# Optimization experiments

Measured on AMD Instinct MI355X. Metric: run time of the kernel, lower is better.

Reference implementation:

```python
import jax, jax.numpy as jnp
import numpy as np

B, S, N, E = 8, 32, 2000, 64000
GH, H = 32, 64  # gat_h, lstm hidden
NEG_SLOPE = 0.2


def setup_inputs() -> dict:
    key = jax.random.key(0)
    ks = jax.random.split(key, 12)
    f32 = jnp.float32
    x = jax.random.normal(ks[0], (B, S, N), f32)
    edge_index = jax.random.randint(ks[1], (2, E), 0, N)
    # GATConv(1, GH, heads=1, concat=False): lin weight [GH,1] -> vector, att_src/att_dst [GH], bias [GH]
    w_lin = jax.random.normal(ks[2], (GH,), f32)
    att_src = jax.random.normal(ks[3], (GH,), f32) * 0.1
    att_dst = jax.random.normal(ks[4], (GH,), f32) * 0.1
    gat_bias = jax.random.normal(ks[5], (GH,), f32) * 0.01
    D = GH * N  # LSTM input size
    W_ih = jax.random.normal(ks[6], (4 * H, D), f32) * (1.0 / np.sqrt(D))
    W_hh = jax.random.normal(ks[7], (4 * H, H), f32) * (1.0 / np.sqrt(H))
    b_ih = jax.random.normal(ks[8], (4 * H,), f32) * 0.01
    b_hh = jax.random.normal(ks[9], (4 * H,), f32) * 0.01
    W_head = jax.random.normal(ks[10], (N, H), f32) * (1.0 / np.sqrt(H))
    b_head = jax.random.normal(ks[11], (N,), f32) * 0.01
    return {"x": x, "edge_index": edge_index, "w_lin": w_lin, "att_src": att_src,
            "att_dst": att_dst, "gat_bias": gat_bias, "W_ih": W_ih, "W_hh": W_hh,
            "b_ih": b_ih, "b_hh": b_hh, "W_head": W_head, "b_head": b_head}


def reference(x, edge_index, w_lin, att_src, att_dst, gat_bias,
              W_ih, W_hh, b_ih, b_hh, W_head, b_head):
    x = x.astype(jnp.float32)
    # --- GAT (in_channels=1, heads=1), batched over (B,S) ---
    # PyG default: add self-loops
    loops = jnp.arange(N)
    ei = jnp.concatenate([edge_index, jnp.stack([loops, loops])], axis=1)
    src, dst = ei[0], ei[1]  # [Et], Et = E + N
    # lifted feature h_n = x_n * w_lin (rank-1), so attention logits are scalar per node
    a_src = x * jnp.dot(w_lin, att_src)  # [B,S,N]
    a_dst = x * jnp.dot(w_lin, att_dst)  # [B,S,N]
    e = jax.nn.leaky_relu(a_src[..., src] + a_dst[..., dst], NEG_SLOPE)  # [B,S,Et]
    e = jnp.moveaxis(e, -1, 0)  # [Et,B,S] (segment axis leading)
    seg_max = jax.ops.segment_max(e, dst, num_segments=N)  # [N,B,S]
    e = jnp.exp(e - seg_max[dst])
    denom = jax.ops.segment_sum(e, dst, num_segments=N)  # [N,B,S]
    alpha = e / denom[dst]  # edge softmax over incoming edges
    x_src = jnp.moveaxis(x[..., src], -1, 0)  # [Et,B,S]
    agg = jax.ops.segment_sum(alpha * x_src, dst, num_segments=N)  # [N,B,S]
    agg = jnp.moveaxis(agg, 0, -1)  # [B,S,N]
    # outer product with w_lin restores [.,GH]; add bias, then relu (from forward)
    h = jax.nn.relu(agg[..., None] * w_lin + gat_bias)  # [B,S,N,GH]
    lstm_in = h.reshape(B, S, N * GH)

    # --- LSTM (1 layer, batch_first), keep final hidden state ---
    def step(carry, xt):
        hp, cp = carry
        gates = xt @ W_ih.T + b_ih + hp @ W_hh.T + b_hh  # [B,4H]
        i, f, g, o = jnp.split(gates, 4, axis=-1)
        c = jax.nn.sigmoid(f) * cp + jax.nn.sigmoid(i) * jnp.tanh(g)
        hn = jax.nn.sigmoid(o) * jnp.tanh(c)
        return (hn, c), None

    h0 = jnp.zeros((B, H), jnp.float32)
    c0 = jnp.zeros((B, H), jnp.float32)
    (hT, _), _ = jax.lax.scan(step, (h0, c0), jnp.swapaxes(lstm_in, 0, 1))
    return hT @ W_head.T + b_head  # [B,N]
```

## Files before the change

kernel.cpp:

```cpp
#include <hip/hip_runtime.h>
#include <hip/hip_bf16.h>
#include <cstddef>
#include <cstdint>

#define B_  8
#define S_  32
#define BT_ 256
#define N_  2000
#define E_  64000
#define GH_ 32
#define H_  64
#define G4_ 256
#define D_  64000
#define NEG_SLOPE_ 0.2f

#define KC_   125
#define NPC_  16

typedef __attribute__((ext_vector_type(8))) short short8;
typedef __attribute__((ext_vector_type(4))) float floatx4;
union U8 { uint32_t u[4]; short8 s; };

__device__ __forceinline__ float fsigmoid(float x) { return 1.0f / (1.0f + __expf(-x)); }
__device__ __forceinline__ float ftanh_(float x)   { return 1.0f - 2.0f / (__expf(2.0f * x) + 1.0f); }

__device__ __forceinline__ void split2(float v0, float v1, uint32_t& hi, uint32_t& lo) {
  uint32_t b0 = __float_as_uint(v0), b1 = __float_as_uint(v1);
  hi = __builtin_amdgcn_perm(b1, b0, 0x07060302u);
  float l0 = v0 - __uint_as_float(b0 & 0xffff0000u);
  float l1 = v1 - __uint_as_float(b1 & 0xffff0000u);
  lo = __builtin_amdgcn_perm(__float_as_uint(l1), __float_as_uint(l0), 0x07060302u);
}


__global__ __launch_bounds__(256) void hist_transpose_kernel(
    const int* __restrict__ ei, int* __restrict__ deg,
    const float* __restrict__ x, float* __restrict__ xT)
{
  const int bid = blockIdx.x;
  const int tid = threadIdx.x;

  if (bid < (E_ + 255) / 256) {
    const int i = bid * 256 + tid;
    if (i < E_) atomicAdd(&deg[ei[E_ + i]], 1);
  }

  __shared__ float tile[32][33];
  const int tx = tid & 31;
  const int ty = tid >> 5;
  const int bx = bid % 63, by = bid / 63;
  const int n0 = bx * 32, bt0 = by * 32;
#pragma unroll
  for (int r = 0; r < 4; ++r) {
    const int nn = n0 + tx;
    if (nn < N_) tile[ty + r * 8][tx] = x[(size_t)(bt0 + ty + r * 8) * N_ + nn];
  }
  __syncthreads();
#pragma unroll
  for (int r = 0; r < 4; ++r) {
    const int n = n0 + ty + r * 8;
    if (n < N_) xT[(size_t)n * BT_ + bt0 + tx] = tile[tx][ty + r * 8];
  }
}

__global__ __launch_bounds__(256) void scan_kernel(
    const int* __restrict__ deg, int* __restrict__ rowptr, int* __restrict__ cursor)
{
  __shared__ int tsum[256];
  const int tid = threadIdx.x;
  int v[8];
  int s = 0;
  const int base = tid * 8;
#pragma unroll
  for (int j = 0; j < 8; ++j) {
    const int idx = base + j;
    const int d = (idx < N_) ? deg[idx] : 0;
    v[j] = s;
    s += d;
  }
  tsum[tid] = s;
  __syncthreads();
  for (int off = 1; off < 256; off <<= 1) {
    int t = 0;
    if (tid >= off) t = tsum[tid - off];
    __syncthreads();
    tsum[tid] += t;
    __syncthreads();
  }
  const int ebase = tsum[tid] - s;
#pragma unroll
  for (int j = 0; j < 8; ++j) {
    const int idx = base + j;
    if (idx < N_) {
      const int r = ebase + v[j];
      rowptr[idx] = r;
      cursor[idx] = r;
    }
  }
  if (tid == 0) rowptr[N_] = E_;
}

__global__ __launch_bounds__(256) void scatter_kernel(
    const int* __restrict__ ei, int* __restrict__ cursor, int* __restrict__ csr_src)
{
  const int i = blockIdx.x * 256 + threadIdx.x;
  if (i >= E_) return;
  const int s = ei[i];
  const int d = ei[E_ + i];
  const int pos = atomicAdd(&cursor[d], 1);
  csr_src[pos] = s;
}

__global__ __launch_bounds__(256) void gat_gather_kernel(
    const float* __restrict__ xT, const int* __restrict__ rowptr,
    const int* __restrict__ csr_src,
    const float* __restrict__ w_lin, const float* __restrict__ att_src,
    const float* __restrict__ att_dst, float* __restrict__ agg_T)
{
  __shared__ int srcs[512];
  const int n   = blockIdx.x;
  const int tid = threadIdx.x;

  float c_s = 0.f, c_d = 0.f;
#pragma unroll
  for (int g = 0; g < GH_; ++g) {
    const float w = w_lin[g];
    c_s += w * att_src[g];
    c_d += w * att_dst[g];
  }

  const int r0 = rowptr[n];
  const int r1 = rowptr[n + 1];
  const int d  = r1 - r0;

  const float xn = xT[(size_t)n * BT_ + tid];
  const float ad = c_d * xn;
  float e = (c_s + c_d) * xn;
  e = e > 0.f ? e : NEG_SLOPE_ * e;
  float w = __expf(e);
  float num = w * xn;
  float den = w;

  for (int base = 0; base < d; base += 512) {
    const int cnt = min(512, d - base);
    __syncthreads();
    for (int i = tid; i < cnt; i += 256) srcs[i] = csr_src[r0 + base + i];
    __syncthreads();

    int p = 0;
    for (; p + 8 <= cnt; p += 8) {
      int   si[8];
      float xi[8];
#pragma unroll
      for (int u = 0; u < 8; ++u) si[u] = srcs[p + u];
#pragma unroll
      for (int u = 0; u < 8; ++u) xi[u] = xT[(size_t)si[u] * BT_ + tid];
#pragma unroll
      for (int u = 0; u < 8; ++u) {
        float ee = fmaf(c_s, xi[u], ad);
        ee = ee > 0.f ? ee : NEG_SLOPE_ * ee;
        const float ww = __expf(ee);
        num = fmaf(ww, xi[u], num);
        den += ww;
      }
    }
    for (; p + 4 <= cnt; p += 4) {
      const int s0 = srcs[p], s1 = srcs[p + 1], s2 = srcs[p + 2], s3 = srcs[p + 3];
      const float x0 = xT[(size_t)s0 * BT_ + tid];
      const float x1 = xT[(size_t)s1 * BT_ + tid];
      const float x2 = xT[(size_t)s2 * BT_ + tid];
      const float x3 = xT[(size_t)s3 * BT_ + tid];
      float e0 = fmaf(c_s, x0, ad); e0 = e0 > 0.f ? e0 : NEG_SLOPE_ * e0;
      float e1 = fmaf(c_s, x1, ad); e1 = e1 > 0.f ? e1 : NEG_SLOPE_ * e1;
      float e2 = fmaf(c_s, x2, ad); e2 = e2 > 0.f ? e2 : NEG_SLOPE_ * e2;
      float e3 = fmaf(c_s, x3, ad); e3 = e3 > 0.f ? e3 : NEG_SLOPE_ * e3;
      const float w0 = __expf(e0), w1 = __expf(e1), w2 = __expf(e2), w3 = __expf(e3);
      num = fmaf(w0, x0, num); den += w0;
      num = fmaf(w1, x1, num); den += w1;
      num = fmaf(w2, x2, num); den += w2;
      num = fmaf(w3, x3, num); den += w3;
    }
    for (; p < cnt; ++p) {
      const int s = srcs[p];
      const float xs = xT[(size_t)s * BT_ + tid];
      float ee = fmaf(c_s, xs, ad);
      ee = ee > 0.f ? ee : NEG_SLOPE_ * ee;
      const float ww = __expf(ee);
      num = fmaf(ww, xs, num);
      den += ww;
    }
  }
  agg_T[(size_t)n * BT_ + tid] = num / den;
}

__global__ __launch_bounds__(256) void gate_mfma_kernel(
    const float* __restrict__ W_ih, const float* __restrict__ agg_T,
    const float* __restrict__ w_lin, const float* __restrict__ gat_bias,
    float* __restrict__ partial, float* __restrict__ pre_gates, int use_atomic)
{
  __shared__ float agg_s[NPC_ * 256];

  const int tid  = threadIdx.x;
  const int nb   = blockIdx.x;
  const int kc   = blockIdx.y;
  const int n0   = kc * NPC_;
  const int wv   = tid >> 6;
  const int lane = tid & 63;
  const int i16  = lane & 15;
  const int q    = lane >> 4;
  const int j0   = nb * 64;

  {
    const float4* src = (const float4*)(agg_T + (size_t)n0 * 256);
    float4* dst = (float4*)agg_s;
#pragma unroll
    for (int p = 0; p < 4; ++p) dst[tid + p * 256] = src[tid + p * 256];
  }

  float wlr[8], gbr[8];
#pragma unroll
  for (int jx = 0; jx < 8; ++jx) {
    wlr[jx] = w_lin[q * 8 + jx];
    gbr[jx] = gat_bias[q * 8 + jx];
  }

  floatx4 acc[4][4];
#pragma unroll
  for (int mt = 0; mt < 4; ++mt)
#pragma unroll
    for (int jt = 0; jt < 4; ++jt)
#pragma unroll
      for (int r = 0; r < 4; ++r) acc[mt][jt][r] = 0.f;

  const float* Wr[4];
#pragma unroll
  for (int jt = 0; jt < 4; ++jt)
    Wr[jt] = W_ih + (size_t)(j0 + jt * 16 + i16) * D_ + (size_t)n0 * GH_ + q * 8;

  float4 cb[8];
#pragma unroll
  for (int jt = 0; jt < 4; ++jt) {
    cb[2 * jt]     = *(const float4*)(Wr[jt]);
    cb[2 * jt + 1] = *(const float4*)(Wr[jt] + 4);
  }

  __syncthreads();

#pragma unroll 1
  for (int nn = 0; nn < NPC_; ++nn) {
    const int nnx = (nn + 1) & (NPC_ - 1);

    short8 ah[4], al[4];
#pragma unroll
    for (int mt = 0; mt < 4; ++mt) {
      const float a = agg_s[nn * 256 + wv * 64 + mt * 16 + i16];
      U8 Hh, Ll;
#pragma unroll
      for (int p = 0; p < 4; ++p) {
        float v0 = fmaf(a, wlr[2 * p],     gbr[2 * p]);
        float v1 = fmaf(a, wlr[2 * p + 1], gbr[2 * p + 1]);
        v0 = fmaxf(v0, 0.f);
        v1 = fmaxf(v1, 0.f);
        split2(v0, v1, Hh.u[p], Ll.u[p]);
      }
      ah[mt] = Hh.s; al[mt] = Ll.s;
    }

#pragma unroll
    for (int jt = 0; jt < 4; ++jt) {
      short8 bh, bl;
      {
        U8 Hh, Ll;
        split2(cb[2 * jt].x,     cb[2 * jt].y,     Hh.u[0], Ll.u[0]);
        split2(cb[2 * jt].z,     cb[2 * jt].w,     Hh.u[1], Ll.u[1]);
        split2(cb[2 * jt + 1].x, cb[2 * jt + 1].y, Hh.u[2], Ll.u[2]);
        split2(cb[2 * jt + 1].z, cb[2 * jt + 1].w, Hh.u[3], Ll.u[3]);
        bh = Hh.s; bl = Ll.s;
      }
      cb[2 * jt]     = *(const float4*)(Wr[jt] + nnx * GH_);
      cb[2 * jt + 1] = *(const float4*)(Wr[jt] + nnx * GH_ + 4);
#pragma unroll
      for (int mt = 0; mt < 4; ++mt) {
        acc[mt][jt] = __builtin_amdgcn_mfma_f32_16x16x32_bf16(ah[mt], bh, acc[mt][jt], 0, 0, 0);
        acc[mt][jt] = __builtin_amdgcn_mfma_f32_16x16x32_bf16(al[mt], bh, acc[mt][jt], 0, 0, 0);
        acc[mt][jt] = __builtin_amdgcn_mfma_f32_16x16x32_bf16(ah[mt], bl, acc[mt][jt], 0, 0, 0);
      }
    }
  }

#pragma unroll
  for (int mt = 0; mt < 4; ++mt) {
    const int bt = wv * 64 + mt * 16 + q * 4;
#pragma unroll
    for (int jt = 0; jt < 4; ++jt) {
      const int j = j0 + jt * 16 + i16;
      if (use_atomic) {
#pragma unroll
        for (int r = 0; r < 4; ++r) atomicAdd(&pre_gates[(bt + r) * G4_ + j], acc[mt][jt][r]);
      } else {
#pragma unroll
        for (int r = 0; r < 4; ++r)
          partial[((size_t)kc * 256 + (bt + r)) * 256 + j] = acc[mt][jt][r];
      }
    }
  }
}

__global__ __launch_bounds__(256) void reduce_kernel(
    const float* __restrict__ partial, float* __restrict__ pre_gates)
{
  const int o = blockIdx.x * 256 + threadIdx.x;
  float s0 = 0.f, s1 = 0.f, s2 = 0.f, s3 = 0.f;
  int kc = 0;
  for (; kc + 4 <= KC_; kc += 4) {
    s0 += partial[(size_t)(kc + 0) * 65536 + o];
    s1 += partial[(size_t)(kc + 1) * 65536 + o];
    s2 += partial[(size_t)(kc + 2) * 65536 + o];
    s3 += partial[(size_t)(kc + 3) * 65536 + o];
  }
  for (; kc < KC_; ++kc) s0 += partial[(size_t)kc * 65536 + o];
  pre_gates[o] = (s0 + s1) + (s2 + s3);
}

__global__ __launch_bounds__(256) void lstm_head_kernel(
    const float* __restrict__ pre_gates, const float* __restrict__ W_hh,
    const float* __restrict__ b_ih, const float* __restrict__ b_hh,
    const float* __restrict__ W_head, const float* __restrict__ b_head,
    float* __restrict__ out)
{
  const int b   = blockIdx.x;
  const int tid = threadIdx.x;
  __shared__ float h_s[H_];
  __shared__ float g_s[G4_];

  float4 wv[16];
  {
    const float4* wrow = (const float4*)(W_hh + (size_t)tid * H_);
#pragma unroll
    for (int q = 0; q < 16; ++q) wv[q] = wrow[q];
  }

  const float bias = b_ih[tid] + b_hh[tid];
  const float* pgp = pre_gates + (size_t)b * S_ * G4_ + tid;
  float pg_cur = pgp[0];
  if (tid < H_) h_s[tid] = 0.f;
  float c = 0.f;
  __syncthreads();

  for (int t = 0; t < S_; ++t) {
    const float pg_nxt = (t + 1 < S_) ? pgp[(size_t)(t + 1) * G4_] : 0.f;

    float g0 = pg_cur + bias, g1 = 0.f, g2 = 0.f, g3 = 0.f;
#pragma unroll
    for (int q = 0; q < 16; ++q) {
      g0 = fmaf(wv[q].x, h_s[4 * q + 0], g0);
      g1 = fmaf(wv[q].y, h_s[4 * q + 1], g1);
      g2 = fmaf(wv[q].z, h_s[4 * q + 2], g2);
      g3 = fmaf(wv[q].w, h_s[4 * q + 3], g3);
    }
    g_s[tid] = (g0 + g1) + (g2 + g3);
    __syncthreads();
    if (tid < H_) {
      const float ig = fsigmoid(g_s[tid]);
      const float fg = fsigmoid(g_s[H_ + tid]);
      const float gg = ftanh_(g_s[2 * H_ + tid]);
      const float og = fsigmoid(g_s[3 * H_ + tid]);
      c = fg * c + ig * gg;
      h_s[tid] = og * ftanh_(c);
    }
    pg_cur = pg_nxt;
    __syncthreads();
  }

  const float4* h4 = (const float4*)h_s;
  for (int n = tid; n < N_; n += 256) {
    const float4* w4 = (const float4*)(W_head + (size_t)n * H_);
    float acc = b_head[n];
#pragma unroll
    for (int q = 0; q < H_ / 4; ++q) {
      const float4 w = w4[q];
      const float4 h = h4[q];
      acc += w.x * h.x + w.y * h.y + w.z * h.z + w.w * h.w;
    }
    out[b * N_ + n] = acc;
  }
}

extern "C" void kernel_launch(void* const* d_in, const int* in_sizes, int n_in,
                              void* d_out, int out_size, void* d_ws, size_t ws_size,
                              hipStream_t stream) {
  const float* x        = (const float*)d_in[0];
  const int*   ei       = (const int*)  d_in[1];
  const float* w_lin    = (const float*)d_in[2];
  const float* att_src  = (const float*)d_in[3];
  const float* att_dst  = (const float*)d_in[4];
  const float* gat_bias = (const float*)d_in[5];
  const float* W_ih     = (const float*)d_in[6];
  const float* W_hh     = (const float*)d_in[7];
  const float* b_ih     = (const float*)d_in[8];
  const float* b_hh     = (const float*)d_in[9];
  const float* W_head   = (const float*)d_in[10];
  const float* b_head   = (const float*)d_in[11];
  float* out = (float*)d_out;

  char* ws = (char*)d_ws;
  float* agg_T     = (float*)(ws + 0);
  float* pre_gates = (float*)(ws + 2048000);
  float* xT        = (float*)(ws + 2312192);
  int*   deg       = (int*)  (ws + 4360192);
  int*   rowptr    = (int*)  (ws + 4368384);
  int*   cursor    = (int*)  (ws + 4376576);
  int*   csr_src   = (int*)  (ws + 4384768);
  float* partial   = (float*)(ws + 4640768);
  const size_t need = 4640768 + (size_t)KC_ * 65536 * sizeof(float);
  const int use_atomic = (ws_size < need) ? 1 : 0;

  hipMemsetAsync(deg, 0, N_ * sizeof(int), stream);
  hist_transpose_kernel<<<dim3(504), dim3(256), 0, stream>>>(ei, deg, x, xT);
  scan_kernel<<<dim3(1), dim3(256), 0, stream>>>(deg, rowptr, cursor);
  scatter_kernel<<<dim3((E_ + 255) / 256), dim3(256), 0, stream>>>(ei, cursor, csr_src);
  gat_gather_kernel<<<dim3(N_), dim3(256), 0, stream>>>(
      xT, rowptr, csr_src, w_lin, att_src, att_dst, agg_T);

  if (use_atomic) {
    hipMemsetAsync(pre_gates, 0, G4_ * BT_ * sizeof(float), stream);
  }
  gate_mfma_kernel<<<dim3(4, KC_), dim3(256), 0, stream>>>(
      W_ih, agg_T, w_lin, gat_bias, partial, pre_gates, use_atomic);
  if (!use_atomic) {
    reduce_kernel<<<dim3(256), dim3(256), 0, stream>>>(partial, pre_gates);
  }

  lstm_head_kernel<<<dim3(B_), dim3(256), 0, stream>>>(
      pre_gates, W_hh, b_ih, b_hh, W_head, b_head, out);
}
```

Baseline: 235.0 us.

## Double-buffer W_ih prefetch, vectorize reduce, split head GEMV into parallel kernel

The gate MFMA loop now keeps two register buffers of W_ih and prefetches two nodes ahead, so global load latency has more time to hide behind MFMA work. The partial-sum reduction reads float4 and launches 64 blocks instead of 256. The output head matvec moves out of the 8-block LSTM kernel into its own kernel that spreads B*N outputs across many blocks, so the head no longer runs on only 8 CUs. This costs extra registers in the gate kernel and one more kernel launch plus a small hT buffer in the workspace.

```diff
diff --git a/kernel.cpp b/kernel.cpp
--- a/kernel.cpp
+++ b/kernel.cpp
@@ -193,6 +193,46 @@
   agg_T[(size_t)n * BT_ + tid] = num / den;
 }
 
+#define GATE_HALF(CURB, NN)                                                    \
+  {                                                                            \
+    const int nnl = ((NN) + 2) & (NPC_ - 1);                                   \
+    short8 ah[4], al[4];                                                       \
+    _Pragma("unroll")                                                          \
+    for (int mt = 0; mt < 4; ++mt) {                                           \
+      const float a = agg_s[(NN) * 256 + wv * 64 + mt * 16 + i16];             \
+      U8 Hh, Ll;                                                               \
+      _Pragma("unroll")                                                        \
+      for (int p = 0; p < 4; ++p) {                                            \
+        float v0 = fmaf(a, wlr[2 * p],     gbr[2 * p]);                        \
+        float v1 = fmaf(a, wlr[2 * p + 1], gbr[2 * p + 1]);                    \
+        v0 = fmaxf(v0, 0.f);                                                   \
+        v1 = fmaxf(v1, 0.f);                                                   \
+        split2(v0, v1, Hh.u[p], Ll.u[p]);                                      \
+      }                                                                        \
+      ah[mt] = Hh.s; al[mt] = Ll.s;                                            \
+    }                                                                          \
+    _Pragma("unroll")                                                          \
+    for (int jt = 0; jt < 4; ++jt) {                                           \
+      short8 bh, bl;                                                           \
+      {                                                                        \
+        U8 Hh, Ll;                                                             \
+        split2(CURB[2 * jt].x,     CURB[2 * jt].y,     Hh.u[0], Ll.u[0]);      \
+        split2(CURB[2 * jt].z,     CURB[2 * jt].w,     Hh.u[1], Ll.u[1]);      \
+        split2(CURB[2 * jt + 1].x, CURB[2 * jt + 1].y, Hh.u[2], Ll.u[2]);      \
+        split2(CURB[2 * jt + 1].z, CURB[2 * jt + 1].w, Hh.u[3], Ll.u[3]);      \
+        bh = Hh.s; bl = Ll.s;                                                  \
+      }                                                                        \
+      CURB[2 * jt]     = *(const float4*)(Wr[jt] + nnl * GH_);                 \
+      CURB[2 * jt + 1] = *(const float4*)(Wr[jt] + nnl * GH_ + 4);             \
+      _Pragma("unroll")                                                        \
+      for (int mt = 0; mt < 4; ++mt) {                                         \
+        acc[mt][jt] = __builtin_amdgcn_mfma_f32_16x16x32_bf16(ah[mt], bh, acc[mt][jt], 0, 0, 0); \
+        acc[mt][jt] = __builtin_amdgcn_mfma_f32_16x16x32_bf16(al[mt], bh, acc[mt][jt], 0, 0, 0); \
+        acc[mt][jt] = __builtin_amdgcn_mfma_f32_16x16x32_bf16(ah[mt], bl, acc[mt][jt], 0, 0, 0); \
+      }                                                                        \
+    }                                                                          \
+  }
+
 __global__ __launch_bounds__(256) void gate_mfma_kernel(
     const float* __restrict__ W_ih, const float* __restrict__ agg_T,
     const float* __restrict__ w_lin, const float* __restrict__ gat_bias,
@@ -237,55 +277,21 @@
   for (int jt = 0; jt < 4; ++jt)
     Wr[jt] = W_ih + (size_t)(j0 + jt * 16 + i16) * D_ + (size_t)n0 * GH_ + q * 8;
 
-  float4 cb[8];
+  float4 cb[8], pb[8];
 #pragma unroll
   for (int jt = 0; jt < 4; ++jt) {
     cb[2 * jt]     = *(const float4*)(Wr[jt]);
     cb[2 * jt + 1] = *(const float4*)(Wr[jt] + 4);
+    pb[2 * jt]     = *(const float4*)(Wr[jt] + GH_);
+    pb[2 * jt + 1] = *(const float4*)(Wr[jt] + GH_ + 4);
   }
 
   __syncthreads();
 
 #pragma unroll 1
-  for (int nn = 0; nn < NPC_; ++nn) {
-    const int nnx = (nn + 1) & (NPC_ - 1);
-
-    short8 ah[4], al[4];
-#pragma unroll
-    for (int mt = 0; mt < 4; ++mt) {
-      const float a = agg_s[nn * 256 + wv * 64 + mt * 16 + i16];
-      U8 Hh, Ll;
-#pragma unroll
-      for (int p = 0; p < 4; ++p) {
-        float v0 = fmaf(a, wlr[2 * p],     gbr[2 * p]);
-        float v1 = fmaf(a, wlr[2 * p + 1], gbr[2 * p + 1]);
-        v0 = fmaxf(v0, 0.f);
-        v1 = fmaxf(v1, 0.f);
-        split2(v0, v1, Hh.u[p], Ll.u[p]);
-      }
-      ah[mt] = Hh.s; al[mt] = Ll.s;
-    }
-
-#pragma unroll
-    for (int jt = 0; jt < 4; ++jt) {
-      short8 bh, bl;
-      {
-        U8 Hh, Ll;
-        split2(cb[2 * jt].x,     cb[2 * jt].y,     Hh.u[0], Ll.u[0]);
-        split2(cb[2 * jt].z,     cb[2 * jt].w,     Hh.u[1], Ll.u[1]);
-        split2(cb[2 * jt + 1].x, cb[2 * jt + 1].y, Hh.u[2], Ll.u[2]);
-        split2(cb[2 * jt + 1].z, cb[2 * jt + 1].w, Hh.u[3], Ll.u[3]);
-        bh = Hh.s; bl = Ll.s;
-      }
-      cb[2 * jt]     = *(const float4*)(Wr[jt] + nnx * GH_);
-      cb[2 * jt + 1] = *(const float4*)(Wr[jt] + nnx * GH_ + 4);
-#pragma unroll
-      for (int mt = 0; mt < 4; ++mt) {
-        acc[mt][jt] = __builtin_amdgcn_mfma_f32_16x16x32_bf16(ah[mt], bh, acc[mt][jt], 0, 0, 0);
-        acc[mt][jt] = __builtin_amdgcn_mfma_f32_16x16x32_bf16(al[mt], bh, acc[mt][jt], 0, 0, 0);
-        acc[mt][jt] = __builtin_amdgcn_mfma_f32_16x16x32_bf16(ah[mt], bl, acc[mt][jt], 0, 0, 0);
-      }
-    }
+  for (int nn = 0; nn < NPC_; nn += 2) {
+    GATE_HALF(cb, nn);
+    GATE_HALF(pb, nn + 1);
   }
 
 #pragma unroll
@@ -309,24 +315,36 @@
 __global__ __launch_bounds__(256) void reduce_kernel(
     const float* __restrict__ partial, float* __restrict__ pre_gates)
 {
-  const int o = blockIdx.x * 256 + threadIdx.x;
-  float s0 = 0.f, s1 = 0.f, s2 = 0.f, s3 = 0.f;
+  const int o4 = blockIdx.x * 256 + threadIdx.x;
+  const float4* p4 = (const float4*)partial;
+  float4 a0 = {0.f, 0.f, 0.f, 0.f}, a1 = a0, a2 = a0, a3 = a0;
   int kc = 0;
   for (; kc + 4 <= KC_; kc += 4) {
-    s0 += partial[(size_t)(kc + 0) * 65536 + o];
-    s1 += partial[(size_t)(kc + 1) * 65536 + o];
-    s2 += partial[(size_t)(kc + 2) * 65536 + o];
-    s3 += partial[(size_t)(kc + 3) * 65536 + o];
-  }
-  for (; kc < KC_; ++kc) s0 += partial[(size_t)kc * 65536 + o];
-  pre_gates[o] = (s0 + s1) + (s2 + s3);
-}
-
-__global__ __launch_bounds__(256) void lstm_head_kernel(
+    const float4 v0 = p4[(size_t)(kc + 0) * 16384 + o4];
+    const float4 v1 = p4[(size_t)(kc + 1) * 16384 + o4];
+    const float4 v2 = p4[(size_t)(kc + 2) * 16384 + o4];
+    const float4 v3 = p4[(size_t)(kc + 3) * 16384 + o4];
+    a0.x += v0.x; a0.y += v0.y; a0.z += v0.z; a0.w += v0.w;
+    a1.x += v1.x; a1.y += v1.y; a1.z += v1.z; a1.w += v1.w;
+    a2.x += v2.x; a2.y += v2.y; a2.z += v2.z; a2.w += v2.w;
+    a3.x += v3.x; a3.y += v3.y; a3.z += v3.z; a3.w += v3.w;
+  }
+  for (; kc < KC_; ++kc) {
+    const float4 v = p4[(size_t)kc * 16384 + o4];
+    a0.x += v.x; a0.y += v.y; a0.z += v.z; a0.w += v.w;
+  }
+  float4 r;
+  r.x = (a0.x + a1.x) + (a2.x + a3.x);
+  r.y = (a0.y + a1.y) + (a2.y + a3.y);
+  r.z = (a0.z + a1.z) + (a2.z + a3.z);
+  r.w = (a0.w + a1.w) + (a2.w + a3.w);
+  ((float4*)pre_gates)[o4] = r;
+}
+
+__global__ __launch_bounds__(256) void lstm_kernel(
     const float* __restrict__ pre_gates, const float* __restrict__ W_hh,
     const float* __restrict__ b_ih, const float* __restrict__ b_hh,
-    const float* __restrict__ W_head, const float* __restrict__ b_head,
-    float* __restrict__ out)
+    float* __restrict__ hT)
 {
   const int b   = blockIdx.x;
   const int tid = threadIdx.x;
@@ -371,19 +389,27 @@
     pg_cur = pg_nxt;
     __syncthreads();
   }
-
-  const float4* h4 = (const float4*)h_s;
-  for (int n = tid; n < N_; n += 256) {
-    const float4* w4 = (const float4*)(W_head + (size_t)n * H_);
-    float acc = b_head[n];
-#pragma unroll
-    for (int q = 0; q < H_ / 4; ++q) {
-      const float4 w = w4[q];
-      const float4 h = h4[q];
-      acc += w.x * h.x + w.y * h.y + w.z * h.z + w.w * h.w;
-    }
-    out[b * N_ + n] = acc;
-  }
+  if (tid < H_) hT[b * H_ + tid] = h_s[tid];
+}
+
+__global__ __launch_bounds__(256) void head_kernel(
+    const float* __restrict__ hT, const float* __restrict__ W_head,
+    const float* __restrict__ b_head, float* __restrict__ out)
+{
+  const int o = blockIdx.x * 256 + threadIdx.x;
+  if (o >= B_ * N_) return;
+  const int b = o / N_;
+  const int n = o - b * N_;
+  const float4* w4 = (const float4*)(W_head + (size_t)n * H_);
+  const float4* h4 = (const float4*)(hT + (size_t)b * H_);
+  float acc = b_head[n];
+#pragma unroll
+  for (int q = 0; q < H_ / 4; ++q) {
+    const float4 w = w4[q];
+    const float4 h = h4[q];
+    acc += w.x * h.x + w.y * h.y + w.z * h.z + w.w * h.w;
+  }
+  out[o] = acc;
 }
 
 extern "C" void kernel_launch(void* const* d_in, const int* in_sizes, int n_in,
@@ -406,6 +432,7 @@
   char* ws = (char*)d_ws;
   float* agg_T     = (float*)(ws + 0);
   float* pre_gates = (float*)(ws + 2048000);
+  float* hT        = (float*)(ws + 2310144);
   float* xT        = (float*)(ws + 2312192);
   int*   deg       = (int*)  (ws + 4360192);
   int*   rowptr    = (int*)  (ws + 4368384);
@@ -428,9 +455,9 @@
   gate_mfma_kernel<<<dim3(4, KC_), dim3(256), 0, stream>>>(
       W_ih, agg_T, w_lin, gat_bias, partial, pre_gates, use_atomic);
   if (!use_atomic) {
-    reduce_kernel<<<dim3(256), dim3(256), 0, stream>>>(partial, pre_gates);
-  }
-
-  lstm_head_kernel<<<dim3(B_), dim3(256), 0, stream>>>(
-      pre_gates, W_hh, b_ih, b_hh, W_head, b_head, out);
-}
+    reduce_kernel<<<dim3(64), dim3(256), 0, stream>>>(partial, pre_gates);
+  }
+
+  lstm_kernel<<<dim3(B_), dim3(256), 0, stream>>>(pre_gates, W_hh, b_ih, b_hh, hT);
+  head_kernel<<<dim3((B_ * N_ + 255) / 256), dim3(256), 0, stream>>>(hT, W_head, b_head, out);
+}
```

New measurement: 226.1 us. -3.8%, faster.
